# Kernel optimization log

Measured on AMD Instinct MI355X. Metric: run time of the kernel, lower is better.

The kernel has to match this reference:

```python
import jax, jax.numpy as jnp
import numpy as np

BS = 8            # block_size
NFA = 0.35        # nfa_threshold
EPS = 1e-08


def setup_inputs() -> dict:
    key = jax.random.key(0)
    k1, k2 = jax.random.split(key)
    B, C, H, W = 16, 3, 512, 512
    ref = jax.random.uniform(k1, (B, C, H, W), dtype=jnp.float32)
    tgt = jax.random.uniform(k2, (B, C, H, W), dtype=jnp.float32)
    return {"ref": ref, "tgt": tgt}


def _luminance(x):
    w = jnp.array([0.299, 0.587, 0.114], dtype=x.dtype).reshape(1, 3, 1, 1)
    return (x * w).sum(axis=1, keepdims=True)  # (B,1,H,W)


def _cross_diffs(img):
    lum = _luminance(img) if img.shape[1] == 3 else img
    e_h = jnp.abs(lum[:, :, :, :-1] - lum[:, :, :, 1:])  # (B,1,H,W-1)
    e_v = jnp.abs(lum[:, :, :-1, :] - lum[:, :, 1:, :])  # (B,1,H-1,W)
    return lum, e_h, e_v


def _phase_mask(de_line_mean, n_lines, out_len, threshold):
    # de_line_mean: (B, n_lines) mean excess energy per line (col or row)
    # Returns (B, out_len) binary mask of boundary lines at winning phase.
    phase = jnp.arange(n_lines) % BS                       # (n_lines,)
    onehot = (phase[:, None] == jnp.arange(BS)[None, :]).astype(de_line_mean.dtype)  # (n_lines, BS)
    counts = onehot.sum(axis=0)                            # (BS,)
    sums = de_line_mean @ onehot                           # (B, BS)
    a_k = sums / counts
    total = de_line_mean.sum(axis=1, keepdims=True)        # (B,1)
    bg = (total - sums) / (n_lines - counts)
    ratio = a_k / (bg + EPS)                               # (B, BS)
    best_k = jnp.argmax(ratio, axis=1)                     # (B,)
    best_r = jnp.max(ratio, axis=1)                        # (B,)
    blocked = best_r > threshold                           # (B,)
    idx = jnp.arange(out_len)
    line_hit = (idx[None, :] % BS == best_k[:, None]) & (idx[None, :] < n_lines)
    return (line_hit & blocked[:, None]).astype(jnp.float32)  # (B, out_len)


def reference(ref, tgt):
    _, e_h_ref, e_v_ref = _cross_diffs(ref)
    lum_t, e_h_tgt, e_v_tgt = _cross_diffs(tgt)
    de_h = jnp.clip(e_h_tgt - e_h_ref, 0.0)  # (B,1,H,W-1)
    de_v = jnp.clip(e_v_tgt - e_v_ref, 0.0)  # (B,1,H-1,W)
    B, _, H, W = lum_t.shape
    threshold = 1.0 / NFA

    col_mean = de_h[:, 0].mean(axis=1)  # (B, W-1): mean over H per column
    row_mean = de_v[:, 0].mean(axis=2)  # (B, H-1): mean over W per row

    mask_h_cols = _phase_mask(col_mean, W - 1, W, threshold)  # (B, W)
    mask_v_rows = _phase_mask(row_mean, H - 1, H, threshold)  # (B, H)

    mask_h = jnp.broadcast_to(mask_h_cols[:, None, None, :], (B, 1, H, W))
    mask_v = jnp.broadcast_to(mask_v_rows[:, None, :, None], (B, 1, H, W))
    return ((mask_h + mask_v) > 0).astype(jnp.float32)
```

## Files before the change

### kernel.cpp

```cpp
#include <hip/hip_runtime.h>

#define BATCH 16
#define HH 512
#define WW 512
#define RSLICE 16
#define NSLICE (HH / RSLICE)

static constexpr size_t PLANE = (size_t)HH * WW;
static constexpr size_t COLP_ELEMS = (size_t)BATCH * NSLICE * WW;
static constexpr size_t ROWS_ELEMS = (size_t)BATCH * HH;

__global__ __launch_bounds__(256) void jbd_reduce(const float* __restrict__ ref,
                                                  const float* __restrict__ tgt,
                                                  float* __restrict__ colp,
                                                  float* __restrict__ rows) {
  const int t = threadIdx.x;
  const int lane = t & 63;
  const int wid = t >> 6;
  const bool bnd = (lane == 63) && (t != 255);
  const int slice = blockIdx.x & (NSLICE - 1);
  const int b = blockIdx.x >> 5;
  const int r0 = slice * RSLICE;
  const float* rb = ref + (size_t)b * 3 * PLANE;
  const float* tb = tgt + (size_t)b * 3 * PLANE;
  __shared__ float rowpart[RSLICE][4];

  float ca0 = 0.f, ca1 = 0.f;
  float pLr0 = 0.f, pLr1 = 0.f, pLt0 = 0.f, pLt1 = 0.f;

  float2 A0, A1, A2, C0, C1, C2;
  float br0 = 0.f, br1 = 0.f, br2 = 0.f, bt0 = 0.f, bt1 = 0.f, bt2 = 0.f;
  {
    const size_t o = (size_t)r0 * WW + 2 * t;
    A0 = *(const float2*)(rb + o);
    A1 = *(const float2*)(rb + o + PLANE);
    A2 = *(const float2*)(rb + o + 2 * PLANE);
    C0 = *(const float2*)(tb + o);
    C1 = *(const float2*)(tb + o + PLANE);
    C2 = *(const float2*)(tb + o + 2 * PLANE);
    if (bnd) {
      const size_t ob = o + 2;
      br0 = rb[ob]; br1 = rb[ob + PLANE]; br2 = rb[ob + 2 * PLANE];
      bt0 = tb[ob]; bt1 = tb[ob + PLANE]; bt2 = tb[ob + 2 * PLANE];
    }
  }
  float2 N0 = A0, N1 = A1, N2 = A2, M0 = C0, M1 = C1, M2 = C2;
  float nbr0 = 0.f, nbr1 = 0.f, nbr2 = 0.f, nbt0 = 0.f, nbt1 = 0.f, nbt2 = 0.f;

#pragma unroll 1
  for (int i = 0; i <= RSLICE; ++i) {
    const int h = r0 + i;
    const bool valid = (h < HH);
    const float lr0 = 0.299f * A0.x + 0.587f * A1.x + 0.114f * A2.x;
    const float lr1 = 0.299f * A0.y + 0.587f * A1.y + 0.114f * A2.y;
    const float lt0 = 0.299f * C0.x + 0.587f * C1.x + 0.114f * C2.x;
    const float lt1 = 0.299f * C0.y + 0.587f * C1.y + 0.114f * C2.y;
    float blr = 0.f, blt = 0.f;
    if (bnd) {
      blr = 0.299f * br0 + 0.587f * br1 + 0.114f * br2;
      blt = 0.299f * bt0 + 0.587f * bt1 + 0.114f * bt2;
    }
    if (i < RSLICE && (h + 1) < HH) {
      const size_t o = (size_t)(h + 1) * WW + 2 * t;
      N0 = *(const float2*)(rb + o);
      N1 = *(const float2*)(rb + o + PLANE);
      N2 = *(const float2*)(rb + o + 2 * PLANE);
      M0 = *(const float2*)(tb + o);
      M1 = *(const float2*)(tb + o + PLANE);
      M2 = *(const float2*)(tb + o + 2 * PLANE);
      if (bnd) {
        const size_t ob = o + 2;
        nbr0 = rb[ob]; nbr1 = rb[ob + PLANE]; nbr2 = rb[ob + 2 * PLANE];
        nbt0 = tb[ob]; nbt1 = tb[ob + PLANE]; nbt2 = tb[ob + 2 * PLANE];
      }
    }
    float nlr = __shfl_down(lr0, 1);
    float nlt = __shfl_down(lt0, 1);
    if (bnd) { nlr = blr; nlt = blt; }
    if (i < RSLICE) {
      ca0 += fmaxf(fabsf(lt0 - lt1) - fabsf(lr0 - lr1), 0.f);
      if (t < 255)
        ca1 += fmaxf(fabsf(lt1 - nlt) - fabsf(lr1 - nlr), 0.f);
    }
    if (i >= 1 && valid) {
      float dv = fmaxf(fabsf(lt0 - pLt0) - fabsf(lr0 - pLr0), 0.f)
               + fmaxf(fabsf(lt1 - pLt1) - fabsf(lr1 - pLr1), 0.f);
      dv += __shfl_xor(dv, 1);
      dv += __shfl_xor(dv, 2);
      dv += __shfl_xor(dv, 4);
      dv += __shfl_xor(dv, 8);
      dv += __shfl_xor(dv, 16);
      dv += __shfl_xor(dv, 32);
      if (lane == 0) rowpart[i - 1][wid] = dv;
    }
    pLr0 = lr0; pLr1 = lr1; pLt0 = lt0; pLt1 = lt1;
    A0 = N0; A1 = N1; A2 = N2; C0 = M0; C1 = M1; C2 = M2;
    br0 = nbr0; br1 = nbr1; br2 = nbr2; bt0 = nbt0; bt1 = nbt1; bt2 = nbt2;
  }
  __syncthreads();
  if (t < RSLICE) {
    const int h = r0 + t;
    if (h < HH - 1)
      rows[(size_t)b * HH + h] =
          rowpart[t][0] + rowpart[t][1] + rowpart[t][2] + rowpart[t][3];
  }
  *(float2*)&colp[((size_t)b * NSLICE + slice) * WW + 2 * t] = make_float2(ca0, ca1);
}

__global__ __launch_bounds__(64) void jbd_phase(const float* __restrict__ colp,
                                                const float* __restrict__ rows,
                                                int* __restrict__ results) {
  const int dir = blockIdx.x & 1;
  const int b = blockIdx.x >> 1;
  const int t = threadIdx.x;
  float s = 0.f;
  if (dir == 0) {
    for (int idx = t; idx < WW - 1; idx += 64) {
      float v = 0.f;
      for (int sl = 0; sl < NSLICE; ++sl)
        v += colp[((size_t)b * NSLICE + sl) * WW + idx];
      s += v;
    }
  } else {
    for (int idx = t; idx < HH - 1; idx += 64)
      s += rows[(size_t)b * HH + idx];
  }
  s *= (1.0f / 512.0f);
  float ps = s;
  ps += __shfl_xor(ps, 8);
  ps += __shfl_xor(ps, 16);
  ps += __shfl_xor(ps, 32);
  float tot = ps;
  tot += __shfl_xor(tot, 1);
  tot += __shfl_xor(tot, 2);
  tot += __shfl_xor(tot, 4);
  const int p = t & 7;
  const float cnt = (p == 7) ? 63.f : 64.f;
  const float a_k = ps / cnt;
  const float bg = (tot - ps) / (511.f - cnt);
  float ratio = a_k / (bg + 1e-8f);
  int bk = p;
  for (int m = 4; m >= 1; m >>= 1) {
    const float ro = __shfl_xor(ratio, m);
    const int ko = __shfl_xor(bk, m);
    if (ro > ratio || (ro == ratio && ko < bk)) { ratio = ro; bk = ko; }
  }
  if (t == 0) {
    const float thr = (float)(1.0 / 0.35);
    results[4 * b + 2 * dir] = bk;
    results[4 * b + 2 * dir + 1] = (ratio > thr) ? 1 : 0;
  }
}

__global__ __launch_bounds__(256) void jbd_write(const int* __restrict__ results,
                                                 float* __restrict__ out) {
  const int idx = blockIdx.x * 256 + threadIdx.x;
  const int b = idx >> 16;
  const int rem = idx & 65535;
  const int h = rem >> 7;
  const int wq = rem & 127;
  const int4 rs = ((const int4*)results)[b];
  const bool rowm = (rs.w != 0) && ((h & 7) == rs.z) && (h < HH - 1);
  float4 o;
  float* po = (float*)&o;
  const int w0 = wq << 2;
#pragma unroll
  for (int j = 0; j < 4; ++j) {
    const int w = w0 + j;
    const bool colm = (rs.y != 0) && ((w & 7) == rs.x) && (w < WW - 1);
    po[j] = (rowm || colm) ? 1.0f : 0.0f;
  }
  ((float4*)out)[idx] = o;
}

extern "C" void kernel_launch(void* const* d_in, const int* in_sizes, int n_in,
                              void* d_out, int out_size, void* d_ws, size_t ws_size,
                              hipStream_t stream) {
  (void)in_sizes; (void)n_in; (void)out_size; (void)ws_size;
  const float* ref = (const float*)d_in[0];
  const float* tgt = (const float*)d_in[1];
  float* colp = (float*)d_ws;
  float* rows = colp + COLP_ELEMS;
  int* results = (int*)(rows + ROWS_ELEMS);
  jbd_reduce<<<BATCH * NSLICE, 256, 0, stream>>>(ref, tgt, colp, rows);
  jbd_phase<<<2 * BATCH, 64, 0, stream>>>(colp, rows, results);
  jbd_write<<<(BATCH * HH * WW / 4) / 256, 256, 0, stream>>>(results, (float*)d_out);
}
```

Before: 137.0 us.

## Widen reduce threads to float4 columns, double-buffer rows, vectorize phase reduction

The reduce kernel now runs 128 threads per block, each handling four columns with float4 loads. Row slices are halved to 8, which doubles the block count, and the rows are prefetched two ahead through an unrolled X/Y double buffer. The phase kernel now reads per-phase column partials with vector loads and reduces each of the 8 phases across the wavefront, replacing the strided scalar loop. The goals are better memory-level parallelism, fewer instructions per byte, and a cheaper final reduction. The cost is more register pressure and twice as many column partials for the phase kernel to sum.

```diff
diff --git a/kernel.cpp b/kernel.cpp
--- a/kernel.cpp
+++ b/kernel.cpp
@@ -3,88 +3,95 @@
 #define BATCH 16
 #define HH 512
 #define WW 512
-#define RSLICE 16
+#define RSLICE 8
 #define NSLICE (HH / RSLICE)
 
 static constexpr size_t PLANE = (size_t)HH * WW;
 static constexpr size_t COLP_ELEMS = (size_t)BATCH * NSLICE * WW;
 static constexpr size_t ROWS_ELEMS = (size_t)BATCH * HH;
 
-__global__ __launch_bounds__(256) void jbd_reduce(const float* __restrict__ ref,
-                                                  const float* __restrict__ tgt,
-                                                  float* __restrict__ colp,
-                                                  float* __restrict__ rows) {
+struct RowBuf {
+  float4 r0, r1, r2, t0, t1, t2;
+  float br0, br1, br2, bt0, bt1, bt2;
+};
+
+__device__ __forceinline__ void load_row(RowBuf& B, const float* __restrict__ rb,
+                                         const float* __restrict__ tb, int row,
+                                         int t, bool bnd) {
+  const size_t o = (size_t)row * WW + 4 * t;
+  B.r0 = *(const float4*)(rb + o);
+  B.r1 = *(const float4*)(rb + o + PLANE);
+  B.r2 = *(const float4*)(rb + o + 2 * PLANE);
+  B.t0 = *(const float4*)(tb + o);
+  B.t1 = *(const float4*)(tb + o + PLANE);
+  B.t2 = *(const float4*)(tb + o + 2 * PLANE);
+  if (bnd) {
+    const size_t ob = o + 4;
+    B.br0 = rb[ob]; B.br1 = rb[ob + PLANE]; B.br2 = rb[ob + 2 * PLANE];
+    B.bt0 = tb[ob]; B.bt1 = tb[ob + PLANE]; B.bt2 = tb[ob + 2 * PLANE];
+  }
+}
+
+__device__ __forceinline__ float lum3(float a, float b, float c) {
+  return 0.299f * a + 0.587f * b + 0.114f * c;
+}
+
+__global__ __launch_bounds__(128, 4) void jbd_reduce(const float* __restrict__ ref,
+                                                     const float* __restrict__ tgt,
+                                                     float* __restrict__ colp,
+                                                     float* __restrict__ rows) {
   const int t = threadIdx.x;
   const int lane = t & 63;
   const int wid = t >> 6;
-  const bool bnd = (lane == 63) && (t != 255);
+  const bool bnd = (t == 63);
   const int slice = blockIdx.x & (NSLICE - 1);
-  const int b = blockIdx.x >> 5;
+  const int b = blockIdx.x >> 6;
   const int r0 = slice * RSLICE;
   const float* rb = ref + (size_t)b * 3 * PLANE;
   const float* tb = tgt + (size_t)b * 3 * PLANE;
-  __shared__ float rowpart[RSLICE][4];
-
-  float ca0 = 0.f, ca1 = 0.f;
-  float pLr0 = 0.f, pLr1 = 0.f, pLt0 = 0.f, pLt1 = 0.f;
-
-  float2 A0, A1, A2, C0, C1, C2;
-  float br0 = 0.f, br1 = 0.f, br2 = 0.f, bt0 = 0.f, bt1 = 0.f, bt2 = 0.f;
-  {
-    const size_t o = (size_t)r0 * WW + 2 * t;
-    A0 = *(const float2*)(rb + o);
-    A1 = *(const float2*)(rb + o + PLANE);
-    A2 = *(const float2*)(rb + o + 2 * PLANE);
-    C0 = *(const float2*)(tb + o);
-    C1 = *(const float2*)(tb + o + PLANE);
-    C2 = *(const float2*)(tb + o + 2 * PLANE);
-    if (bnd) {
-      const size_t ob = o + 2;
-      br0 = rb[ob]; br1 = rb[ob + PLANE]; br2 = rb[ob + 2 * PLANE];
-      bt0 = tb[ob]; bt1 = tb[ob + PLANE]; bt2 = tb[ob + 2 * PLANE];
-    }
-  }
-  float2 N0 = A0, N1 = A1, N2 = A2, M0 = C0, M1 = C1, M2 = C2;
-  float nbr0 = 0.f, nbr1 = 0.f, nbr2 = 0.f, nbt0 = 0.f, nbt1 = 0.f, nbt2 = 0.f;
-
-#pragma unroll 1
+  __shared__ float rowpart[RSLICE][2];
+
+  float ca0 = 0.f, ca1 = 0.f, ca2 = 0.f, ca3 = 0.f;
+  float plr0 = 0.f, plr1 = 0.f, plr2 = 0.f, plr3 = 0.f;
+  float plt0 = 0.f, plt1 = 0.f, plt2 = 0.f, plt3 = 0.f;
+
+  RowBuf X, Y;
+  load_row(X, rb, tb, r0, t, bnd);
+  load_row(Y, rb, tb, r0 + 1, t, bnd);
+
+#pragma unroll
   for (int i = 0; i <= RSLICE; ++i) {
-    const int h = r0 + i;
-    const bool valid = (h < HH);
-    const float lr0 = 0.299f * A0.x + 0.587f * A1.x + 0.114f * A2.x;
-    const float lr1 = 0.299f * A0.y + 0.587f * A1.y + 0.114f * A2.y;
-    const float lt0 = 0.299f * C0.x + 0.587f * C1.x + 0.114f * C2.x;
-    const float lt1 = 0.299f * C0.y + 0.587f * C1.y + 0.114f * C2.y;
+    RowBuf& C = (i & 1) ? Y : X;
+    const float a0 = lum3(C.r0.x, C.r1.x, C.r2.x);
+    const float a1 = lum3(C.r0.y, C.r1.y, C.r2.y);
+    const float a2 = lum3(C.r0.z, C.r1.z, C.r2.z);
+    const float a3 = lum3(C.r0.w, C.r1.w, C.r2.w);
+    const float c0 = lum3(C.t0.x, C.t1.x, C.t2.x);
+    const float c1 = lum3(C.t0.y, C.t1.y, C.t2.y);
+    const float c2 = lum3(C.t0.z, C.t1.z, C.t2.z);
+    const float c3 = lum3(C.t0.w, C.t1.w, C.t2.w);
     float blr = 0.f, blt = 0.f;
     if (bnd) {
-      blr = 0.299f * br0 + 0.587f * br1 + 0.114f * br2;
-      blt = 0.299f * bt0 + 0.587f * bt1 + 0.114f * bt2;
-    }
-    if (i < RSLICE && (h + 1) < HH) {
-      const size_t o = (size_t)(h + 1) * WW + 2 * t;
-      N0 = *(const float2*)(rb + o);
-      N1 = *(const float2*)(rb + o + PLANE);
-      N2 = *(const float2*)(rb + o + 2 * PLANE);
-      M0 = *(const float2*)(tb + o);
-      M1 = *(const float2*)(tb + o + PLANE);
-      M2 = *(const float2*)(tb + o + 2 * PLANE);
-      if (bnd) {
-        const size_t ob = o + 2;
-        nbr0 = rb[ob]; nbr1 = rb[ob + PLANE]; nbr2 = rb[ob + 2 * PLANE];
-        nbt0 = tb[ob]; nbt1 = tb[ob + PLANE]; nbt2 = tb[ob + 2 * PLANE];
-      }
-    }
-    float nlr = __shfl_down(lr0, 1);
-    float nlt = __shfl_down(lt0, 1);
+      blr = lum3(C.br0, C.br1, C.br2);
+      blt = lum3(C.bt0, C.bt1, C.bt2);
+    }
+    if (i + 2 <= RSLICE)
+      load_row(C, rb, tb, min(r0 + i + 2, HH - 1), t, bnd);
+    float nlr = __shfl_down(a0, 1);
+    float nlt = __shfl_down(c0, 1);
     if (bnd) { nlr = blr; nlt = blt; }
     if (i < RSLICE) {
-      ca0 += fmaxf(fabsf(lt0 - lt1) - fabsf(lr0 - lr1), 0.f);
-      if (t < 255)
-        ca1 += fmaxf(fabsf(lt1 - nlt) - fabsf(lr1 - nlr), 0.f);
-    }
-    if (i >= 1 && valid) {
-      float dv = fmaxf(fabsf(lt0 - pLt0) - fabsf(lr0 - pLr0), 0.f)
-               + fmaxf(fabsf(lt1 - pLt1) - fabsf(lr1 - pLr1), 0.f);
+      ca0 += fmaxf(fabsf(c0 - c1) - fabsf(a0 - a1), 0.f);
+      ca1 += fmaxf(fabsf(c1 - c2) - fabsf(a1 - a2), 0.f);
+      ca2 += fmaxf(fabsf(c2 - c3) - fabsf(a2 - a3), 0.f);
+      if (t < 127)
+        ca3 += fmaxf(fabsf(c3 - nlt) - fabsf(a3 - nlr), 0.f);
+    }
+    if (i >= 1 && (r0 + i) < HH) {
+      float dv = fmaxf(fabsf(c0 - plt0) - fabsf(a0 - plr0), 0.f)
+               + fmaxf(fabsf(c1 - plt1) - fabsf(a1 - plr1), 0.f)
+               + fmaxf(fabsf(c2 - plt2) - fabsf(a2 - plr2), 0.f)
+               + fmaxf(fabsf(c3 - plt3) - fabsf(a3 - plr3), 0.f);
       dv += __shfl_xor(dv, 1);
       dv += __shfl_xor(dv, 2);
       dv += __shfl_xor(dv, 4);
@@ -93,18 +100,17 @@
       dv += __shfl_xor(dv, 32);
       if (lane == 0) rowpart[i - 1][wid] = dv;
     }
-    pLr0 = lr0; pLr1 = lr1; pLt0 = lt0; pLt1 = lt1;
-    A0 = N0; A1 = N1; A2 = N2; C0 = M0; C1 = M1; C2 = M2;
-    br0 = nbr0; br1 = nbr1; br2 = nbr2; bt0 = nbt0; bt1 = nbt1; bt2 = nbt2;
+    plr0 = a0; plr1 = a1; plr2 = a2; plr3 = a3;
+    plt0 = c0; plt1 = c1; plt2 = c2; plt3 = c3;
   }
   __syncthreads();
   if (t < RSLICE) {
     const int h = r0 + t;
     if (h < HH - 1)
-      rows[(size_t)b * HH + h] =
-          rowpart[t][0] + rowpart[t][1] + rowpart[t][2] + rowpart[t][3];
-  }
-  *(float2*)&colp[((size_t)b * NSLICE + slice) * WW + 2 * t] = make_float2(ca0, ca1);
+      rows[(size_t)b * HH + h] = rowpart[t][0] + rowpart[t][1];
+  }
+  *(float4*)&colp[((size_t)b * NSLICE + slice) * WW + 4 * t] =
+      make_float4(ca0, ca1, ca2, ca3);
 }
 
 __global__ __launch_bounds__(64) void jbd_phase(const float* __restrict__ colp,
@@ -113,42 +119,53 @@
   const int dir = blockIdx.x & 1;
   const int b = blockIdx.x >> 1;
   const int t = threadIdx.x;
-  float s = 0.f;
+  float c0 = 0.f, c1 = 0.f, c2 = 0.f, c3 = 0.f;
+  float c4 = 0.f, c5 = 0.f, c6 = 0.f, c7 = 0.f;
   if (dir == 0) {
-    for (int idx = t; idx < WW - 1; idx += 64) {
-      float v = 0.f;
-      for (int sl = 0; sl < NSLICE; ++sl)
-        v += colp[((size_t)b * NSLICE + sl) * WW + idx];
-      s += v;
+#pragma unroll 4
+    for (int sl = 0; sl < NSLICE; ++sl) {
+      const float* p = colp + ((size_t)b * NSLICE + sl) * WW + 8 * t;
+      const float4 u = *(const float4*)p;
+      const float4 v = *(const float4*)(p + 4);
+      c0 += u.x; c1 += u.y; c2 += u.z; c3 += u.w;
+      c4 += v.x; c5 += v.y; c6 += v.z; c7 += v.w;
     }
   } else {
-    for (int idx = t; idx < HH - 1; idx += 64)
-      s += rows[(size_t)b * HH + idx];
-  }
-  s *= (1.0f / 512.0f);
-  float ps = s;
-  ps += __shfl_xor(ps, 8);
-  ps += __shfl_xor(ps, 16);
-  ps += __shfl_xor(ps, 32);
-  float tot = ps;
-  tot += __shfl_xor(tot, 1);
-  tot += __shfl_xor(tot, 2);
-  tot += __shfl_xor(tot, 4);
-  const int p = t & 7;
-  const float cnt = (p == 7) ? 63.f : 64.f;
-  const float a_k = ps / cnt;
-  const float bg = (tot - ps) / (511.f - cnt);
-  float ratio = a_k / (bg + 1e-8f);
-  int bk = p;
-  for (int m = 4; m >= 1; m >>= 1) {
-    const float ro = __shfl_xor(ratio, m);
-    const int ko = __shfl_xor(bk, m);
-    if (ro > ratio || (ro == ratio && ko < bk)) { ratio = ro; bk = ko; }
+    const float* p = rows + (size_t)b * HH + 8 * t;
+    const float4 u = *(const float4*)p;
+    const float4 v = *(const float4*)(p + 4);
+    c0 = u.x; c1 = u.y; c2 = u.z; c3 = u.w;
+    c4 = v.x; c5 = v.y; c6 = v.z; c7 = v.w;
+  }
+  if (t == 63) c7 = 0.f;
+  float ps[8] = {c0, c1, c2, c3, c4, c5, c6, c7};
+  float tot = 0.f;
+#pragma unroll
+  for (int p = 0; p < 8; ++p) {
+    float v = ps[p];
+    v += __shfl_xor(v, 1);
+    v += __shfl_xor(v, 2);
+    v += __shfl_xor(v, 4);
+    v += __shfl_xor(v, 8);
+    v += __shfl_xor(v, 16);
+    v += __shfl_xor(v, 32);
+    v *= (1.0f / 512.0f);
+    ps[p] = v;
+    tot += v;
+  }
+  float best = -1.f;
+  int bk = 0;
+#pragma unroll
+  for (int p = 0; p < 8; ++p) {
+    const float cnt = (p == 7) ? 63.f : 64.f;
+    const float a_k = ps[p] / cnt;
+    const float bg = (tot - ps[p]) / (511.f - cnt);
+    const float r = a_k / (bg + 1e-8f);
+    if (r > best) { best = r; bk = p; }
   }
   if (t == 0) {
-    const float thr = (float)(1.0 / 0.35);
     results[4 * b + 2 * dir] = bk;
-    results[4 * b + 2 * dir + 1] = (ratio > thr) ? 1 : 0;
+    results[4 * b + 2 * dir + 1] = (best > (float)(1.0 / 0.35)) ? 1 : 0;
   }
 }
 
@@ -182,7 +199,7 @@
   float* colp = (float*)d_ws;
   float* rows = colp + COLP_ELEMS;
   int* results = (int*)(rows + ROWS_ELEMS);
-  jbd_reduce<<<BATCH * NSLICE, 256, 0, stream>>>(ref, tgt, colp, rows);
+  jbd_reduce<<<BATCH * NSLICE, 128, 0, stream>>>(ref, tgt, colp, rows);
   jbd_phase<<<2 * BATCH, 64, 0, stream>>>(colp, rows, results);
   jbd_write<<<(BATCH * HH * WW / 4) / 256, 256, 0, stream>>>(results, (float*)d_out);
 }
```

New measurement: 172.3 us. +25.7%, slower.
